# Kernel optimization log

Measured on AMD Instinct MI355X. Metric: run time of the kernel, lower is better.

The kernel has to match this reference:

```python
import jax, jax.numpy as jnp
import numpy as np

D = 64            # number of devices (leaves hold D/8 each)
B = 65536         # batch of states
FEAT = 5 + 4 * D  # 261
HID = 128


def setup_inputs() -> dict:
    key = jax.random.key(0)
    ks = jax.random.split(key, 10)
    def nrm(k, shape, s=0.1):
        return jax.random.normal(k, shape, jnp.float32) * s
    return {
        "x": jax.random.normal(ks[0], (B, FEAT), jnp.float32),
        # gate params per depth d: 2^d nodes, weight dim 5 + 4*D/2^d
        "w0": nrm(ks[1], (1, 5 + 4 * D)),
        "b0": jnp.zeros((1,), jnp.float32),
        "w1": nrm(ks[2], (2, 5 + 4 * (D // 2))),
        "b1": jnp.zeros((2,), jnp.float32),
        "w2": nrm(ks[3], (4, 5 + 4 * (D // 4))),
        "b2": jnp.zeros((4,), jnp.float32),
        # leaf prob_dist (torch inits to zeros; random here for a non-trivial baseline)
        "leaf_probs": nrm(ks[4], (8, D // 8), 1.0),
        # critic MLP
        "Wc1": nrm(ks[5], (FEAT, HID)),
        "bc1": jnp.zeros((HID,), jnp.float32),
        "Wc2": nrm(ks[6], (HID, 1)),
        "bc2": jnp.zeros((1,), jnp.float32),
    }


def reference(x, w0, b0, w1, b1, w2, b2, leaf_probs, Wc1, bc1, Wc2, bc2):
    # Batched deterministic ClusterTree routing (exploration disabled).
    x5 = x[:, :5]                       # (B, 5) global features
    dev = x[:, 5:].reshape(B, D, 4)     # (B, D, 4) per-device features
    node = jnp.zeros((B,), jnp.int32)   # current node index at each depth
    cum = jnp.ones((B,), x.dtype)       # product of gate values along path
    for d, (wd, bd) in enumerate([(w0, b0), (w1, b1), (w2, b2)]):
        nd = D >> d                     # devices per node at this depth
        off = node * nd                 # contiguous-cluster start offset
        idx = off[:, None] + jnp.arange(nd)                     # (B, nd)
        dslice = jnp.take_along_axis(dev, idx[:, :, None], 1)   # (B, nd, 4)
        w = wd[node]                    # (B, 5 + 4*nd)
        gate = (jnp.sum(x5 * w[:, :5], -1)
                + jnp.sum(dslice.reshape(B, -1) * w[:, 5:], -1)
                + bd[node])
        val = jax.nn.sigmoid(gate)
        cum = cum * val                 # torch: val * child_output, recursively
        node = node * 2 + (val >= 0.5).astype(jnp.int32)
    p = cum[:, None] * leaf_probs[node]                 # (B, D//8)
    v = jax.nn.relu(x @ Wc1 + bc1) @ Wc2 + bc2          # (B, 1) critic
    return p, v
```

## Files before the change

kernel.cpp:

```cpp
#include <hip/hip_runtime.h>
#include <hip/hip_bf16.h>
#include <stdint.h>

#define NB    65536
#define FEATN 261
#define HIDN  128
#define NSTEP 17
#define SROW  296

#define ROWSG 128
#define NTHRG 512

typedef __attribute__((ext_vector_type(8)))  short bf16x8;
typedef __attribute__((ext_vector_type(16))) float f32x16;
typedef float f32x4u __attribute__((ext_vector_type(4), aligned(4)));

#define MFMA32(A, B, C) __builtin_amdgcn_mfma_f32_32x32x16_bf16(A, B, C, 0, 0, 0)

__device__ __forceinline__ uint16_t f2b(float v) {
    __hip_bfloat16 b = __float2bfloat16(v);
    return *reinterpret_cast<uint16_t*>(&b);
}

__global__ void tree_kernel(
    const float* __restrict__ x,
    const float* __restrict__ w0, const float* __restrict__ b0,
    const float* __restrict__ w1, const float* __restrict__ b1,
    const float* __restrict__ w2, const float* __restrict__ b2,
    const float* __restrict__ leaf,
    const float* __restrict__ Wc1, uint16_t* __restrict__ wsB,
    float* __restrict__ out_p)
{
    const int tid = threadIdx.x;

    if (blockIdx.x < 17) {
        int t = blockIdx.x * 256 + tid;
        if (t < NSTEP * 4 * 64) {
            int p = t >> 6, l = t & 63;
            int s = p >> 2, nt = p & 3;
            int n = nt * 32 + (l & 31);
            int kb = 16 * s + 8 * (l >> 5);
            uint16_t hw[8];
            #pragma unroll
            for (int j = 0; j < 8; ++j) {
                int k = kb + j;
                float v = (k < FEATN) ? Wc1[(size_t)k * HIDN + n] : 0.f;
                hw[j] = f2b(v);
            }
            *reinterpret_cast<uint4*>(wsB + (size_t)p * 512 + l * 8) =
                *reinterpret_cast<uint4*>(hw);
        }
    }

    const int s   = tid & 15;
    const int row = blockIdx.x * 16 + (tid >> 4);
    const float* xr = x + (size_t)row * FEATN;

    f32x4u w0q[4];
    #pragma unroll
    for (int j = 0; j < 4; ++j)
        w0q[j] = *reinterpret_cast<const f32x4u*>(w0 + 4 * s + 64 * j);
    const float w0t = (s < 5) ? w0[256 + s] : 0.f;

    f32x4u w1aq[2], w1bq[2];
    #pragma unroll
    for (int j = 0; j < 2; ++j) {
        w1aq[j] = *reinterpret_cast<const f32x4u*>(w1 + 5 + 8 * s + 4 * j);
        w1bq[j] = *reinterpret_cast<const f32x4u*>(w1 + 133 + 5 + 8 * s + 4 * j);
    }
    const float w1a5 = (s < 5) ? w1[s]       : 0.f;
    const float w1b5 = (s < 5) ? w1[133 + s] : 0.f;

    f32x4u w2q0 = *reinterpret_cast<const f32x4u*>(w2 +  0 * 69 + 5 + 4 * s);
    f32x4u w2q1 = *reinterpret_cast<const f32x4u*>(w2 +  1 * 69 + 5 + 4 * s);
    f32x4u w2q2 = *reinterpret_cast<const f32x4u*>(w2 +  2 * 69 + 5 + 4 * s);
    f32x4u w2q3 = *reinterpret_cast<const f32x4u*>(w2 +  3 * 69 + 5 + 4 * s);
    float w25_0 = (s < 5) ? w2[0 * 69 + s] : 0.f;
    float w25_1 = (s < 5) ? w2[1 * 69 + s] : 0.f;
    float w25_2 = (s < 5) ? w2[2 * 69 + s] : 0.f;
    float w25_3 = (s < 5) ? w2[3 * 69 + s] : 0.f;

    f32x4u xq[4];
    #pragma unroll
    for (int j = 0; j < 4; ++j)
        xq[j] = *reinterpret_cast<const f32x4u*>(xr + 4 * s + 64 * j);
    const float xt  = (s < 5) ? xr[256 + s] : 0.f;
    const float xs5 = (s < 5) ? xr[s]       : 0.f;

    float part = xt * w0t;
    #pragma unroll
    for (int j = 0; j < 4; ++j)
        #pragma unroll
        for (int c = 0; c < 4; ++c)
            part += xq[j][c] * w0q[j][c];
    part += __shfl_xor(part, 1);
    part += __shfl_xor(part, 2);
    part += __shfl_xor(part, 4);
    part += __shfl_xor(part, 8);
    float gate = part + b0[0];
    int node = (gate >= 0.f) ? 1 : 0;
    float cum = 1.f / (1.f + __expf(-gate));

    {
        const float* base = xr + 5 + 128 * node + 8 * s;
        f32x4u xw0 = *reinterpret_cast<const f32x4u*>(base);
        f32x4u xw1 = *reinterpret_cast<const f32x4u*>(base + 4);
        part = xs5 * (node ? w1b5 : w1a5);
        #pragma unroll
        for (int c = 0; c < 4; ++c) {
            part += xw0[c] * (node ? w1bq[0][c] : w1aq[0][c]);
            part += xw1[c] * (node ? w1bq[1][c] : w1aq[1][c]);
        }
        part += __shfl_xor(part, 1);
        part += __shfl_xor(part, 2);
        part += __shfl_xor(part, 4);
        part += __shfl_xor(part, 8);
        gate = part + b1[node];
        cum *= 1.f / (1.f + __expf(-gate));
        node = node * 2 + ((gate >= 0.f) ? 1 : 0);
    }
    {
        f32x4u xv2 = *reinterpret_cast<const f32x4u*>(xr + 5 + 64 * node + 4 * s);
        f32x4u t0 = (node & 1) ? w2q1 : w2q0;
        f32x4u t1 = (node & 1) ? w2q3 : w2q2;
        f32x4u wsel = (node & 2) ? t1 : t0;
        float w5a = (node & 1) ? w25_1 : w25_0;
        float w5b = (node & 1) ? w25_3 : w25_2;
        float w5sel = (node & 2) ? w5b : w5a;
        part = xs5 * w5sel;
        #pragma unroll
        for (int c = 0; c < 4; ++c) part += xv2[c] * wsel[c];
        part += __shfl_xor(part, 1);
        part += __shfl_xor(part, 2);
        part += __shfl_xor(part, 4);
        part += __shfl_xor(part, 8);
        gate = part + b2[node];
        cum *= 1.f / (1.f + __expf(-gate));
        node = node * 2 + ((gate >= 0.f) ? 1 : 0);
    }
    if (s < 8)
        out_p[(size_t)row * 8 + s] = cum * leaf[node * 8 + s];
}

__global__ __launch_bounds__(NTHRG, 2) void critic_gemm(
    const float* __restrict__ x,
    const uint16_t* __restrict__ wsB,
    const float* __restrict__ bc1, const float* __restrict__ Wc2,
    const float* __restrict__ bc2,
    float* __restrict__ out_v)
{
    __shared__ uint16_t Axs[ROWSG * SROW];
    __shared__ float bc1s[HIDN];
    __shared__ float wc2s[HIDN];
    __shared__ float vpart[ROWSG * 2];

    const int tid = threadIdx.x;
    const int rowBase = blockIdx.x * ROWSG;

    if (tid < HIDN) { bc1s[tid] = bc1[tid]; wc2s[tid] = Wc2[tid]; }
    if (tid < ROWSG) {
        uint16_t* rp = Axs + tid * SROW;
        rp[261] = 0;
        *reinterpret_cast<uint32_t*>(rp + 262) = 0u;
        uint4 z; z.x = z.y = z.z = z.w = 0u;
        *reinterpret_cast<uint4*>(rp + 264) = z;
        *reinterpret_cast<uint4*>(rp + 272) = z;
        *reinterpret_cast<uint4*>(rp + 280) = z;
        *reinterpret_cast<uint4*>(rp + 288) = z;
    }

    {
        for (int idx = tid; idx < ROWSG * 66; idx += NTHRG) {
            int row = idx / 66;
            int seg = idx - row * 66;
            const float* src = x + (size_t)(rowBase + row) * FEATN + 4 * seg;
            uint16_t* dst = Axs + row * SROW + 4 * seg;
            if (seg < 65) {
                f32x4u v = *reinterpret_cast<const f32x4u*>(src);
                uint32_t p0 = (uint32_t)f2b(v[0]) | ((uint32_t)f2b(v[1]) << 16);
                uint32_t p1 = (uint32_t)f2b(v[2]) | ((uint32_t)f2b(v[3]) << 16);
                uint2 pk; pk.x = p0; pk.y = p1;
                *reinterpret_cast<uint2*>(dst) = pk;
            } else {
                dst[0] = f2b(src[0]);
            }
        }
    }
    __syncthreads();

    const int lane = tid & 63;
    const int w    = tid >> 6;
    const int mt   = w >> 1;
    const int nh   = w & 1;

    const uint16_t* arow = Axs + (mt * 32 + (lane & 31)) * SROW + (lane >> 5) * 8;
    const uint16_t* bgl  = wsB + (size_t)(2 * nh) * 512 + lane * 8;

    bf16x8 af[NSTEP], bf0[NSTEP], bf1[NSTEP];
    #pragma unroll
    for (int s = 0; s < NSTEP; ++s) {
        af[s]  = *reinterpret_cast<const bf16x8*>(arow + s * 16);
        bf0[s] = *reinterpret_cast<const bf16x8*>(bgl + (size_t)(s * 4)     * 512);
        bf1[s] = *reinterpret_cast<const bf16x8*>(bgl + (size_t)(s * 4 + 1) * 512);
    }

    f32x16 acc0 = {}, acc1 = {};
    #pragma unroll
    for (int s = 0; s < NSTEP; ++s) {
        acc0 = MFMA32(af[s], bf0[s], acc0);
        acc1 = MFMA32(af[s], bf1[s], acc1);
    }

    {
        const int c = lane & 31;
        const int q = lane >> 5;
        const int n0 = 2 * nh * 32 + c;
        const int n1 = n0 + 32;
        const float bb0 = bc1s[n0], ww0 = wc2s[n0];
        const float bb1 = bc1s[n1], ww1 = wc2s[n1];

        float pv[16];
        #pragma unroll
        for (int reg = 0; reg < 16; ++reg) {
            float h0 = acc0[reg] + bb0; h0 = h0 > 0.f ? h0 : 0.f;
            float h1 = acc1[reg] + bb1; h1 = h1 > 0.f ? h1 : 0.f;
            float t = h0 * ww0 + h1 * ww1;
            t += __shfl_xor(t, 1);
            t += __shfl_xor(t, 2);
            t += __shfl_xor(t, 4);
            t += __shfl_xor(t, 8);
            t += __shfl_xor(t, 16);
            pv[reg] = t;
        }
        #pragma unroll
        for (int reg = 0; reg < 16; ++reg) {
            if (c == reg) {
                int row_local = (reg & 3) + 8 * (reg >> 2) + 4 * q;
                vpart[(mt * 32 + row_local) * 2 + nh] = pv[reg];
            }
        }
    }
    __syncthreads();
    if (tid < ROWSG)
        out_v[rowBase + tid] = vpart[tid * 2] + vpart[tid * 2 + 1] + bc2[0];
}

extern "C" void kernel_launch(void* const* d_in, const int* in_sizes, int n_in,
                              void* d_out, int out_size, void* d_ws, size_t ws_size,
                              hipStream_t stream) {
    const float* x    = (const float*)d_in[0];
    const float* w0   = (const float*)d_in[1];
    const float* b0   = (const float*)d_in[2];
    const float* w1   = (const float*)d_in[3];
    const float* b1   = (const float*)d_in[4];
    const float* w2   = (const float*)d_in[5];
    const float* b2   = (const float*)d_in[6];
    const float* leaf = (const float*)d_in[7];
    const float* Wc1  = (const float*)d_in[8];
    const float* bc1  = (const float*)d_in[9];
    const float* Wc2  = (const float*)d_in[10];
    const float* bc2  = (const float*)d_in[11];

    uint16_t* wsB = (uint16_t*)d_ws;

    float* out_p = (float*)d_out;
    float* out_v = out_p + (size_t)NB * 8;

    tree_kernel<<<NB / 16, 256, 0, stream>>>(
        x, w0, b0, w1, b1, w2, b2, leaf, Wc1, wsB, out_p);
    critic_gemm<<<NB / ROWSG, NTHRG, 0, stream>>>(
        x, wsB, bc1, Wc2, bc2, out_v);
}
```

Before: 135.2 us.

## Fuse tree routing and critic GEMM into one kernel with separate weight prep

After: 147.0 us. 1.09x slower.

```diff
diff --git a/kernel.cpp b/kernel.cpp
--- a/kernel.cpp
+++ b/kernel.cpp
@@ -8,8 +8,8 @@
 #define NSTEP 17
 #define SROW  296
 
-#define ROWSG 128
-#define NTHRG 512
+#define ROWSF 64
+#define NTHRF 256
 
 typedef __attribute__((ext_vector_type(8)))  short bf16x8;
 typedef __attribute__((ext_vector_type(16))) float f32x16;
@@ -22,143 +22,48 @@
     return *reinterpret_cast<uint16_t*>(&b);
 }
 
-__global__ void tree_kernel(
+__global__ void prep_kernel(const float* __restrict__ Wc1,
+                            uint16_t* __restrict__ wsB)
+{
+    int t = blockIdx.x * 256 + threadIdx.x;
+    if (t < NSTEP * 4 * 64) {
+        int p = t >> 6, l = t & 63;
+        int s = p >> 2, nt = p & 3;
+        int n = nt * 32 + (l & 31);
+        int kb = 16 * s + 8 * (l >> 5);
+        uint16_t hw[8];
+        #pragma unroll
+        for (int j = 0; j < 8; ++j) {
+            int k = kb + j;
+            float v = (k < FEATN) ? Wc1[(size_t)k * HIDN + n] : 0.f;
+            hw[j] = f2b(v);
+        }
+        *reinterpret_cast<uint4*>(wsB + (size_t)p * 512 + l * 8) =
+            *reinterpret_cast<uint4*>(hw);
+    }
+}
+
+__global__ __launch_bounds__(NTHRF, 4) void fused_kernel(
     const float* __restrict__ x,
     const float* __restrict__ w0, const float* __restrict__ b0,
     const float* __restrict__ w1, const float* __restrict__ b1,
     const float* __restrict__ w2, const float* __restrict__ b2,
     const float* __restrict__ leaf,
-    const float* __restrict__ Wc1, uint16_t* __restrict__ wsB,
-    float* __restrict__ out_p)
-{
-    const int tid = threadIdx.x;
-
-    if (blockIdx.x < 17) {
-        int t = blockIdx.x * 256 + tid;
-        if (t < NSTEP * 4 * 64) {
-            int p = t >> 6, l = t & 63;
-            int s = p >> 2, nt = p & 3;
-            int n = nt * 32 + (l & 31);
-            int kb = 16 * s + 8 * (l >> 5);
-            uint16_t hw[8];
-            #pragma unroll
-            for (int j = 0; j < 8; ++j) {
-                int k = kb + j;
-                float v = (k < FEATN) ? Wc1[(size_t)k * HIDN + n] : 0.f;
-                hw[j] = f2b(v);
-            }
-            *reinterpret_cast<uint4*>(wsB + (size_t)p * 512 + l * 8) =
-                *reinterpret_cast<uint4*>(hw);
-        }
-    }
-
-    const int s   = tid & 15;
-    const int row = blockIdx.x * 16 + (tid >> 4);
-    const float* xr = x + (size_t)row * FEATN;
-
-    f32x4u w0q[4];
-    #pragma unroll
-    for (int j = 0; j < 4; ++j)
-        w0q[j] = *reinterpret_cast<const f32x4u*>(w0 + 4 * s + 64 * j);
-    const float w0t = (s < 5) ? w0[256 + s] : 0.f;
-
-    f32x4u w1aq[2], w1bq[2];
-    #pragma unroll
-    for (int j = 0; j < 2; ++j) {
-        w1aq[j] = *reinterpret_cast<const f32x4u*>(w1 + 5 + 8 * s + 4 * j);
-        w1bq[j] = *reinterpret_cast<const f32x4u*>(w1 + 133 + 5 + 8 * s + 4 * j);
-    }
-    const float w1a5 = (s < 5) ? w1[s]       : 0.f;
-    const float w1b5 = (s < 5) ? w1[133 + s] : 0.f;
-
-    f32x4u w2q0 = *reinterpret_cast<const f32x4u*>(w2 +  0 * 69 + 5 + 4 * s);
-    f32x4u w2q1 = *reinterpret_cast<const f32x4u*>(w2 +  1 * 69 + 5 + 4 * s);
-    f32x4u w2q2 = *reinterpret_cast<const f32x4u*>(w2 +  2 * 69 + 5 + 4 * s);
-    f32x4u w2q3 = *reinterpret_cast<const f32x4u*>(w2 +  3 * 69 + 5 + 4 * s);
-    float w25_0 = (s < 5) ? w2[0 * 69 + s] : 0.f;
-    float w25_1 = (s < 5) ? w2[1 * 69 + s] : 0.f;
-    float w25_2 = (s < 5) ? w2[2 * 69 + s] : 0.f;
-    float w25_3 = (s < 5) ? w2[3 * 69 + s] : 0.f;
-
-    f32x4u xq[4];
-    #pragma unroll
-    for (int j = 0; j < 4; ++j)
-        xq[j] = *reinterpret_cast<const f32x4u*>(xr + 4 * s + 64 * j);
-    const float xt  = (s < 5) ? xr[256 + s] : 0.f;
-    const float xs5 = (s < 5) ? xr[s]       : 0.f;
-
-    float part = xt * w0t;
-    #pragma unroll
-    for (int j = 0; j < 4; ++j)
-        #pragma unroll
-        for (int c = 0; c < 4; ++c)
-            part += xq[j][c] * w0q[j][c];
-    part += __shfl_xor(part, 1);
-    part += __shfl_xor(part, 2);
-    part += __shfl_xor(part, 4);
-    part += __shfl_xor(part, 8);
-    float gate = part + b0[0];
-    int node = (gate >= 0.f) ? 1 : 0;
-    float cum = 1.f / (1.f + __expf(-gate));
-
-    {
-        const float* base = xr + 5 + 128 * node + 8 * s;
-        f32x4u xw0 = *reinterpret_cast<const f32x4u*>(base);
-        f32x4u xw1 = *reinterpret_cast<const f32x4u*>(base + 4);
-        part = xs5 * (node ? w1b5 : w1a5);
-        #pragma unroll
-        for (int c = 0; c < 4; ++c) {
-            part += xw0[c] * (node ? w1bq[0][c] : w1aq[0][c]);
-            part += xw1[c] * (node ? w1bq[1][c] : w1aq[1][c]);
-        }
-        part += __shfl_xor(part, 1);
-        part += __shfl_xor(part, 2);
-        part += __shfl_xor(part, 4);
-        part += __shfl_xor(part, 8);
-        gate = part + b1[node];
-        cum *= 1.f / (1.f + __expf(-gate));
-        node = node * 2 + ((gate >= 0.f) ? 1 : 0);
-    }
-    {
-        f32x4u xv2 = *reinterpret_cast<const f32x4u*>(xr + 5 + 64 * node + 4 * s);
-        f32x4u t0 = (node & 1) ? w2q1 : w2q0;
-        f32x4u t1 = (node & 1) ? w2q3 : w2q2;
-        f32x4u wsel = (node & 2) ? t1 : t0;
-        float w5a = (node & 1) ? w25_1 : w25_0;
-        float w5b = (node & 1) ? w25_3 : w25_2;
-        float w5sel = (node & 2) ? w5b : w5a;
-        part = xs5 * w5sel;
-        #pragma unroll
-        for (int c = 0; c < 4; ++c) part += xv2[c] * wsel[c];
-        part += __shfl_xor(part, 1);
-        part += __shfl_xor(part, 2);
-        part += __shfl_xor(part, 4);
-        part += __shfl_xor(part, 8);
-        gate = part + b2[node];
-        cum *= 1.f / (1.f + __expf(-gate));
-        node = node * 2 + ((gate >= 0.f) ? 1 : 0);
-    }
-    if (s < 8)
-        out_p[(size_t)row * 8 + s] = cum * leaf[node * 8 + s];
-}
-
-__global__ __launch_bounds__(NTHRG, 2) void critic_gemm(
-    const float* __restrict__ x,
     const uint16_t* __restrict__ wsB,
     const float* __restrict__ bc1, const float* __restrict__ Wc2,
     const float* __restrict__ bc2,
-    float* __restrict__ out_v)
+    float* __restrict__ out_p, float* __restrict__ out_v)
 {
-    __shared__ uint16_t Axs[ROWSG * SROW];
+    __shared__ uint16_t Axs[ROWSF * SROW];
     __shared__ float bc1s[HIDN];
     __shared__ float wc2s[HIDN];
-    __shared__ float vpart[ROWSG * 2];
+    __shared__ float vpart[ROWSF * 2];
 
     const int tid = threadIdx.x;
-    const int rowBase = blockIdx.x * ROWSG;
+    const int rowBase = blockIdx.x * ROWSF;
 
     if (tid < HIDN) { bc1s[tid] = bc1[tid]; wc2s[tid] = Wc2[tid]; }
-    if (tid < ROWSG) {
+    if (tid < ROWSF) {
         uint16_t* rp = Axs + tid * SROW;
         rp[261] = 0;
         *reinterpret_cast<uint32_t*>(rp + 262) = 0u;
@@ -169,23 +74,118 @@
         *reinterpret_cast<uint4*>(rp + 288) = z;
     }
 
+    for (int idx = tid; idx < ROWSF * 66; idx += NTHRF) {
+        int row = idx / 66;
+        int seg = idx - row * 66;
+        const float* src = x + (size_t)(rowBase + row) * FEATN + 4 * seg;
+        uint16_t* dst = Axs + row * SROW + 4 * seg;
+        if (seg < 65) {
+            f32x4u v = *reinterpret_cast<const f32x4u*>(src);
+            uint32_t p0 = (uint32_t)f2b(v[0]) | ((uint32_t)f2b(v[1]) << 16);
+            uint32_t p1 = (uint32_t)f2b(v[2]) | ((uint32_t)f2b(v[3]) << 16);
+            uint2 pk; pk.x = p0; pk.y = p1;
+            *reinterpret_cast<uint2*>(dst) = pk;
+        } else {
+            dst[0] = f2b(src[0]);
+        }
+    }
+
     {
-        for (int idx = tid; idx < ROWSG * 66; idx += NTHRG) {
-            int row = idx / 66;
-            int seg = idx - row * 66;
-            const float* src = x + (size_t)(rowBase + row) * FEATN + 4 * seg;
-            uint16_t* dst = Axs + row * SROW + 4 * seg;
-            if (seg < 65) {
-                f32x4u v = *reinterpret_cast<const f32x4u*>(src);
-                uint32_t p0 = (uint32_t)f2b(v[0]) | ((uint32_t)f2b(v[1]) << 16);
-                uint32_t p1 = (uint32_t)f2b(v[2]) | ((uint32_t)f2b(v[3]) << 16);
-                uint2 pk; pk.x = p0; pk.y = p1;
-                *reinterpret_cast<uint2*>(dst) = pk;
-            } else {
-                dst[0] = f2b(src[0]);
+        const int s = tid & 15;
+        const int g = tid >> 4;
+
+        f32x4u w0q[4];
+        #pragma unroll
+        for (int j = 0; j < 4; ++j)
+            w0q[j] = *reinterpret_cast<const f32x4u*>(w0 + 4 * s + 64 * j);
+        const float w0t = (s < 5) ? w0[256 + s] : 0.f;
+
+        f32x4u w1aq[2], w1bq[2];
+        #pragma unroll
+        for (int j = 0; j < 2; ++j) {
+            w1aq[j] = *reinterpret_cast<const f32x4u*>(w1 + 5 + 8 * s + 4 * j);
+            w1bq[j] = *reinterpret_cast<const f32x4u*>(w1 + 133 + 5 + 8 * s + 4 * j);
+        }
+        const float w1a5 = (s < 5) ? w1[s]       : 0.f;
+        const float w1b5 = (s < 5) ? w1[133 + s] : 0.f;
+
+        f32x4u w2q0 = *reinterpret_cast<const f32x4u*>(w2 +  0 * 69 + 5 + 4 * s);
+        f32x4u w2q1 = *reinterpret_cast<const f32x4u*>(w2 +  1 * 69 + 5 + 4 * s);
+        f32x4u w2q2 = *reinterpret_cast<const f32x4u*>(w2 +  2 * 69 + 5 + 4 * s);
+        f32x4u w2q3 = *reinterpret_cast<const f32x4u*>(w2 +  3 * 69 + 5 + 4 * s);
+        const float w25_0 = (s < 5) ? w2[0 * 69 + s] : 0.f;
+        const float w25_1 = (s < 5) ? w2[1 * 69 + s] : 0.f;
+        const float w25_2 = (s < 5) ? w2[2 * 69 + s] : 0.f;
+        const float w25_3 = (s < 5) ? w2[3 * 69 + s] : 0.f;
+
+        #pragma unroll 1
+        for (int r4 = 0; r4 < 4; ++r4) {
+            const int row = rowBase + r4 * 16 + g;
+            const float* xr = x + (size_t)row * FEATN;
+
+            f32x4u xq[4];
+            #pragma unroll
+            for (int j = 0; j < 4; ++j)
+                xq[j] = *reinterpret_cast<const f32x4u*>(xr + 4 * s + 64 * j);
+            const float xt  = (s < 5) ? xr[256 + s] : 0.f;
+            const float xs5 = (s < 5) ? xr[s]       : 0.f;
+
+            float part = xt * w0t;
+            #pragma unroll
+            for (int j = 0; j < 4; ++j)
+                #pragma unroll
+                for (int c = 0; c < 4; ++c)
+                    part += xq[j][c] * w0q[j][c];
+            part += __shfl_xor(part, 1);
+            part += __shfl_xor(part, 2);
+            part += __shfl_xor(part, 4);
+            part += __shfl_xor(part, 8);
+            float gate = part + b0[0];
+            int node = (gate >= 0.f) ? 1 : 0;
+            float cum = 1.f / (1.f + __expf(-gate));
+
+            {
+                const float* base = xr + 5 + 128 * node + 8 * s;
+                f32x4u xw0 = *reinterpret_cast<const f32x4u*>(base);
+                f32x4u xw1 = *reinterpret_cast<const f32x4u*>(base + 4);
+                part = xs5 * (node ? w1b5 : w1a5);
+                #pragma unroll
+                for (int c = 0; c < 4; ++c) {
+                    part += xw0[c] * (node ? w1bq[0][c] : w1aq[0][c]);
+                    part += xw1[c] * (node ? w1bq[1][c] : w1aq[1][c]);
+                }
+                part += __shfl_xor(part, 1);
+                part += __shfl_xor(part, 2);
+                part += __shfl_xor(part, 4);
+                part += __shfl_xor(part, 8);
+                gate = part + b1[node];
+                cum *= 1.f / (1.f + __expf(-gate));
+                node = node * 2 + ((gate >= 0.f) ? 1 : 0);
             }
-        }
-    }
+            {
+                f32x4u xv2 = *reinterpret_cast<const f32x4u*>(xr + 5 + 64 * node + 4 * s);
+                f32x4u t0 = (node & 1) ? w2q1 : w2q0;
+                f32x4u t1 = (node & 1) ? w2q3 : w2q2;
+                f32x4u wsel = (node & 2) ? t1 : t0;
+                float w5a = (node & 1) ? w25_1 : w25_0;
+                float w5b = (node & 1) ? w25_3 : w25_2;
+                float w5sel = (node & 2) ? w5b : w5a;
+                part = xs5 * w5sel;
+                #pragma unroll
+                for (int c = 0; c < 4; ++c) part += xv2[c] * wsel[c];
+                part += __shfl_xor(part, 1);
+                part += __shfl_xor(part, 2);
+                part += __shfl_xor(part, 4);
+                part += __shfl_xor(part, 8);
+                gate = part + b2[node];
+                cum *= 1.f / (1.f + __expf(-gate));
+                node = node * 2 + ((gate >= 0.f) ? 1 : 0);
+            }
+            if (s < 8)
+                out_p[(size_t)row * 8 + s] = cum * leaf[node * 8 + s];
+        }
+    }
+
     __syncthreads();
 
     const int lane = tid & 63;
@@ -196,19 +196,14 @@
     const uint16_t* arow = Axs + (mt * 32 + (lane & 31)) * SROW + (lane >> 5) * 8;
     const uint16_t* bgl  = wsB + (size_t)(2 * nh) * 512 + lane * 8;
 
-    bf16x8 af[NSTEP], bf0[NSTEP], bf1[NSTEP];
-    #pragma unroll
-    for (int s = 0; s < NSTEP; ++s) {
-        af[s]  = *reinterpret_cast<const bf16x8*>(arow + s * 16);
-        bf0[s] = *reinterpret_cast<const bf16x8*>(bgl + (size_t)(s * 4)     * 512);
-        bf1[s] = *reinterpret_cast<const bf16x8*>(bgl + (size_t)(s * 4 + 1) * 512);
-    }
-
     f32x16 acc0 = {}, acc1 = {};
     #pragma unroll
-    for (int s = 0; s < NSTEP; ++s) {
-        acc0 = MFMA32(af[s], bf0[s], acc0);
-        acc1 = MFMA32(af[s], bf1[s], acc1);
+    for (int ss = 0; ss < NSTEP; ++ss) {
+        bf16x8 af  = *reinterpret_cast<const bf16x8*>(arow + ss * 16);
+        bf16x8 bf0 = *reinterpret_cast<const bf16x8*>(bgl + (size_t)(ss * 4)     * 512);
+        bf16x8 bf1 = *reinterpret_cast<const bf16x8*>(bgl + (size_t)(ss * 4 + 1) * 512);
+        acc0 = MFMA32(af, bf0, acc0);
+        acc1 = MFMA32(af, bf1, acc1);
     }
 
     {
@@ -241,7 +236,7 @@
         }
     }
     __syncthreads();
-    if (tid < ROWSG)
+    if (tid < ROWSF)
         out_v[rowBase + tid] = vpart[tid * 2] + vpart[tid * 2 + 1] + bc2[0];
 }
 
@@ -266,8 +261,7 @@
     float* out_p = (float*)d_out;
     float* out_v = out_p + (size_t)NB * 8;
 
-    tree_kernel<<<NB / 16, 256, 0, stream>>>(
-        x, w0, b0, w1, b1, w2, b2, leaf, Wc1, wsB, out_p);
-    critic_gemm<<<NB / ROWSG, NTHRG, 0, stream>>>(
-        x, wsB, bc1, Wc2, bc2, out_v);
-}
+    prep_kernel<<<17, 256, 0, stream>>>(Wc1, wsB);
+    fused_kernel<<<NB / ROWSF, NTHRF, 0, stream>>>(
+        x, w0, b0, w1, b1, w2, b2, leaf, wsB, bc1, Wc2, bc2, out_p, out_v);
+}
```
